# Performance work log

Hardware: AMD Instinct MI355X
Metric: run time of the kernel (lower is better)

## Reference

```python
import jax, jax.numpy as jnp
import numpy as np

NB, NG = 131072, 32768            # n_bus, n_gen nodes
EBB, EGB, EBG = 2097152, 65536, 65536  # bus-bus, gen->bus, bus->gen edges
CIN, C, COUT = 32, 64, 32         # in_channels, n_channels, out_channels
NL, NT = 2, 5                     # n_layers, n_taps+1
EPS = 1e-5


def setup_inputs() -> dict:
    key = jax.random.key(0)
    ks = iter(jax.random.split(key, 40))
    rn = lambda shape, s=1.0: jax.random.normal(next(ks), shape, dtype=jnp.float32) * s
    ri = lambda shape, hi: jax.random.randint(next(ks), shape, 0, hi, dtype=jnp.int32)
    inp = {
        'x_bus': rn((NB, CIN)), 'x_gen': rn((NG, CIN)),
        'readin_W_bus': rn((CIN, C), CIN ** -0.5), 'readin_b_bus': jnp.zeros((C,), jnp.float32),
        'readin_W_gen': rn((CIN, C), CIN ** -0.5), 'readin_b_gen': jnp.zeros((C,), jnp.float32),
        'bn_gamma_bus': jnp.ones((NL, C), jnp.float32), 'bn_beta_bus': jnp.zeros((NL, C), jnp.float32),
        'bn_gamma_gen': jnp.ones((NL, C), jnp.float32), 'bn_beta_gen': jnp.zeros((NL, C), jnp.float32),
        'taps_W_bus': rn((NL, NT, C, C), C ** -0.5), 'taps_b_bus': jnp.zeros((NL, NT, C), jnp.float32),
        'taps_W_gen': rn((NL, NT, C, C), C ** -0.5), 'taps_b_gen': jnp.zeros((NL, NT, C), jnp.float32),
        'readout_W_bus': rn((C, COUT), C ** -0.5), 'readout_b_bus': jnp.zeros((COUT,), jnp.float32),
        'readout_W_gen': rn((C, COUT), C ** -0.5), 'readout_b_gen': jnp.zeros((COUT,), jnp.float32),
        'edge_bb': ri((2, EBB), NB),
        'edge_gb_src': ri((EGB,), NG), 'edge_gb_dst': ri((EGB,), NB),
        'edge_bg_src': ri((EBG,), NB), 'edge_bg_dst': ri((EBG,), NG),
    }
    return inp


def _lrelu(v):
    return jnp.where(v >= 0, v, 0.01 * v)  # nn.LeakyReLU default slope


def _bn(v, g, b):
    # training-mode BatchNorm over the node dimension (biased variance)
    m = jnp.mean(v, axis=0)
    s = jnp.var(v, axis=0)
    return (v - m) * jax.lax.rsqrt(s + EPS) * g + b


def reference(x_bus, x_gen,
              readin_W_bus, readin_b_bus, readin_W_gen, readin_b_gen,
              bn_gamma_bus, bn_beta_bus, bn_gamma_gen, bn_beta_gen,
              taps_W_bus, taps_b_bus, taps_W_gen, taps_b_gen,
              readout_W_bus, readout_b_bus, readout_W_gen, readout_b_gen,
              edge_bb, edge_gb_src, edge_gb_dst, edge_bg_src, edge_bg_dst):
    seg = jax.ops.segment_sum
    bbs, bbd = edge_bb[0], edge_bb[1]
    # readin (single HeteroDictLinear, plain_last)
    xb = x_bus @ readin_W_bus + readin_b_bus   # [NB, C]
    xg = x_gen @ readin_W_gen + readin_b_gen   # [NG, C]
    for l in range(NL):  # residual blocks: norm -> act -> (dropout p=0) -> graph filter -> +x
        yb = _lrelu(_bn(xb, bn_gamma_bus[l], bn_beta_bus[l]))
        yg = _lrelu(_bn(xg, bn_gamma_gen[l], bn_beta_gen[l]))
        zb = yb @ taps_W_bus[l, 0] + taps_b_bus[l, 0]
        zg = yg @ taps_W_gen[l, 0] + taps_b_gen[l, 0]
        cb, cg = yb, yg
        for k in range(1, NT):  # graph shift (scatter-add over hetero edges) + per-type tap
            nb = seg(cb[bbs], bbd, num_segments=NB) + seg(cg[edge_gb_src], edge_gb_dst, num_segments=NB)
            ng = seg(cb[edge_bg_src], edge_bg_dst, num_segments=NG)
            cb, cg = nb, ng
            zb = zb + cb @ taps_W_bus[l, k] + taps_b_bus[l, k]
            zg = zg + cg @ taps_W_gen[l, k] + taps_b_gen[l, k]
        xb = xb + zb
        xg = xg + zg
    out_b = xb @ readout_W_bus + readout_b_bus  # [NB, COUT]
    out_g = xg @ readout_W_gen + readout_b_gen  # [NG, COUT]
    return (out_b, out_g)
```

## Files before the change

kernel.cpp:

```cpp
#include <hip/hip_runtime.h>

#define NBUS 131072
#define NGEN 32768
#define NALL (NBUS + NGEN)
#define NEBB 2097152
#define NEGB 65536
#define NEBG 65536
#define NEBUS (NEBB + NEGB)
#define NTILE (NALL / 64)
#define NTILE_BUS (NBUS / 64)

typedef float f32x2 __attribute__((ext_vector_type(2)));
typedef float f32x4 __attribute__((ext_vector_type(4)));
typedef short s16x8 __attribute__((ext_vector_type(8)));
typedef unsigned short u16;

__device__ inline f32x2 bf2x2(unsigned v) {
  f32x2 r;
  r.x = __builtin_bit_cast(float, v << 16);
  r.y = __builtin_bit_cast(float, v & 0xFFFF0000u);
  return r;
}
__device__ inline u16 f2bf(float f) {
  unsigned u = __builtin_bit_cast(unsigned, f);
  unsigned r = u + 0x7FFFu + ((u >> 16) & 1u);
  return (u16)(r >> 16);
}
__device__ inline unsigned pack2bf(float a, float b) {
  return (unsigned)f2bf(a) | ((unsigned)f2bf(b) << 16);
}

__global__ void __launch_bounds__(256) k_convw(const float* __restrict__ tWb,
                                               const float* __restrict__ tWg,
                                               const float* __restrict__ roWb,
                                               const float* __restrict__ roWg,
                                               const float* __restrict__ riWb,
                                               const float* __restrict__ riWg,
                                               u16* __restrict__ wt,
                                               u16* __restrict__ rot,
                                               u16* __restrict__ riwt) {
  int t = blockIdx.x * 256 + threadIdx.x;
  int S = gridDim.x * 256;
  for (int i = t; i < 20 * 4096; i += S) {
    int mat = i >> 12, off = i & 4095, n = off >> 6, k = off & 63;
    const float* src = (mat < 10) ? tWb : tWg;
    int tap = (mat < 10) ? mat : mat - 10;
    wt[i] = f2bf(src[(size_t)tap * 4096 + k * 64 + n]);
  }
  for (int i = t; i < 2 * 2048; i += S) {
    int type = i >> 11, off = i & 2047, n = off >> 6, k = off & 63;
    const float* src = type ? roWg : roWb;
    rot[i] = f2bf(src[k * 32 + n]);
  }
  for (int i = t; i < 2 * 2048; i += S) {
    int type = i >> 11, off = i & 2047, n = off >> 5, k = off & 31;
    const float* src = type ? riWg : riWb;
    riwt[i] = f2bf(src[k * 64 + n]);
  }
}

__global__ void __launch_bounds__(256) k_hist_sl(const int* __restrict__ bbDst,
                                                 const int* __restrict__ gbDst,
                                                 const int* __restrict__ bgDst,
                                                 int* __restrict__ busCnt,
                                                 int* __restrict__ bgCnt) {
  const int g = blockIdx.x & 7;
  const int blk = blockIdx.x >> 3;
  const int nblk = gridDim.x >> 3;
  const int start = blk * 256 + threadIdx.x;
  const int S = nblk * 256;
  int i = start;
  for (; i + 3 * S < NEBB; i += 4 * S) {
    int d0 = bbDst[i], d1 = bbDst[i + S], d2 = bbDst[i + 2 * S], d3 = bbDst[i + 3 * S];
    if ((d0 >> 14) == g) atomicAdd(&busCnt[d0], 1);
    if ((d1 >> 14) == g) atomicAdd(&busCnt[d1], 1);
    if ((d2 >> 14) == g) atomicAdd(&busCnt[d2], 1);
    if ((d3 >> 14) == g) atomicAdd(&busCnt[d3], 1);
  }
  for (; i < NEBB; i += S) {
    int d = bbDst[i];
    if ((d >> 14) == g) atomicAdd(&busCnt[d], 1);
  }
  for (i = start; i < NEGB; i += S) {
    int d = gbDst[i];
    if ((d >> 14) == g) atomicAdd(&busCnt[d], 1);
  }
  for (i = start; i < NEBG; i += S) {
    int d = bgDst[i];
    if ((d >> 12) == g) atomicAdd(&bgCnt[d], 1);
  }
}

__global__ void k_scan1(const int* __restrict__ in, int* __restrict__ out,
                        int* __restrict__ bsums, int n) {
  __shared__ int sh[256];
  int t = threadIdx.x;
  int base = blockIdx.x * 1024 + t * 4;
  int v0 = (base + 0 < n) ? in[base + 0] : 0;
  int v1 = (base + 1 < n) ? in[base + 1] : 0;
  int v2 = (base + 2 < n) ? in[base + 2] : 0;
  int v3 = (base + 3 < n) ? in[base + 3] : 0;
  int t0 = v0, t1 = t0 + v1, t2 = t1 + v2, t3 = t2 + v3;
  sh[t] = t3;
  __syncthreads();
  for (int off = 1; off < 256; off <<= 1) {
    int x = (t >= off) ? sh[t - off] : 0;
    __syncthreads();
    sh[t] += x;
    __syncthreads();
  }
  int excl = (t > 0) ? sh[t - 1] : 0;
  if (base + 0 < n) out[base + 0] = excl;
  if (base + 1 < n) out[base + 1] = excl + t0;
  if (base + 2 < n) out[base + 2] = excl + t1;
  if (base + 3 < n) out[base + 3] = excl + t2;
  if (t == 255) bsums[blockIdx.x] = sh[255];
}

__global__ void k_scan2(int* __restrict__ bsums, int nb) {
  __shared__ int sh[256];
  int t = threadIdx.x;
  int v = (t < nb) ? bsums[t] : 0;
  sh[t] = v;
  __syncthreads();
  for (int off = 1; off < 256; off <<= 1) {
    int x = (t >= off) ? sh[t - off] : 0;
    __syncthreads();
    sh[t] += x;
    __syncthreads();
  }
  int excl = (t > 0) ? sh[t - 1] : 0;
  if (t < nb) bsums[t] = excl;
}

__global__ void k_scan3(int* __restrict__ off, int* __restrict__ cur,
                        const int* __restrict__ bsums, int n, int E) {
  int stride = gridDim.x * blockDim.x;
  for (int i = blockIdx.x * blockDim.x + threadIdx.x; i < n; i += stride) {
    int o = off[i] + bsums[i >> 10];
    off[i] = o;
    cur[i] = o;
  }
  if (blockIdx.x == 0 && threadIdx.x == 0) off[n] = E;
}

__global__ void __launch_bounds__(256) k_fill_sl(const int* __restrict__ bbSrc,
                                                 const int* __restrict__ bbDst,
                                                 const int* __restrict__ gbSrc,
                                                 const int* __restrict__ gbDst,
                                                 const int* __restrict__ bgSrc,
                                                 const int* __restrict__ bgDst,
                                                 int* __restrict__ busCur,
                                                 int* __restrict__ bgCur,
                                                 int* __restrict__ busSrt,
                                                 int* __restrict__ bgSrt) {
  const int g = blockIdx.x & 7;
  const int tid = threadIdx.x;
  if (blockIdx.x < 2048) {
    const int blk = blockIdx.x >> 3;
    const int S = 256 * 256;
    int i = blk * 256 + tid;
    for (; i + 3 * S < NEBB; i += 4 * S) {
      int d0 = bbDst[i], d1 = bbDst[i + S], d2 = bbDst[i + 2 * S], d3 = bbDst[i + 3 * S];
      if ((d0 >> 14) == g) { int p = atomicAdd(&busCur[d0], 1); busSrt[p] = bbSrc[i]; }
      if ((d1 >> 14) == g) { int p = atomicAdd(&busCur[d1], 1); busSrt[p] = bbSrc[i + S]; }
      if ((d2 >> 14) == g) { int p = atomicAdd(&busCur[d2], 1); busSrt[p] = bbSrc[i + 2 * S]; }
      if ((d3 >> 14) == g) { int p = atomicAdd(&busCur[d3], 1); busSrt[p] = bbSrc[i + 3 * S]; }
    }
    for (; i < NEBB; i += S) {
      int d = bbDst[i];
      if ((d >> 14) == g) { int p = atomicAdd(&busCur[d], 1); busSrt[p] = bbSrc[i]; }
    }
  } else if (blockIdx.x < 2304) {
    const int blk = (blockIdx.x - 2048) >> 3;
    const int S = 32 * 256;
    for (int i = blk * 256 + tid; i < NEGB; i += S) {
      int d = gbDst[i];
      if ((d >> 14) == g) { int p = atomicAdd(&busCur[d], 1); busSrt[p] = gbSrc[i] + NBUS; }
    }
  } else {
    const int blk = (blockIdx.x - 2304) >> 3;
    const int S = 32 * 256;
    for (int i = blk * 256 + tid; i < NEBG; i += S) {
      int d = bgDst[i];
      if ((d >> 12) == g) { int p = atomicAdd(&bgCur[d], 1); bgSrt[p] = bgSrc[i]; }
    }
  }
}

__global__ void __launch_bounds__(256) k_readin(const float* __restrict__ xbus,
                                                const float* __restrict__ xgen,
                                                const u16* __restrict__ riwt,
                                                const float* __restrict__ bb_,
                                                const float* __restrict__ bg_,
                                                float* __restrict__ y,
                                                float* __restrict__ stats) {
  __shared__ float sst[128];
  const int tile = blockIdx.x;
  const bool isBus = tile < NTILE_BUS;
  const int tid = threadIdx.x, lane = tid & 63, wv = tid >> 6;
  const int m = lane & 15, kq = lane >> 4;
  const int grow = tile * 64 + wv * 16 + m;
  const float* xp = isBus ? &xbus[(size_t)grow * 32] : &xgen[(size_t)(grow - NBUS) * 32];
  s16x8 a;
#pragma unroll
  for (int j = 0; j < 8; j++) a[j] = (short)f2bf(xp[kq * 8 + j]);
  const u16* rb = riwt + (size_t)(isBus ? 0 : 1) * 2048;
  const float* bb = isBus ? bb_ : bg_;
  f32x4 acc[4];
#pragma unroll
  for (int cb = 0; cb < 4; cb++) {
    acc[cb] = (f32x4){0.f, 0.f, 0.f, 0.f};
    const u16* wp = rb + (cb * 16 + m) * 32 + kq * 8;
    s16x8 b = *(const s16x8*)wp;
    acc[cb] = __builtin_amdgcn_mfma_f32_16x16x32_bf16(a, b, acc[cb], 0, 0, 0);
  }
  if (tid < 128) sst[tid] = 0.f;
  __syncthreads();
  const int orow0 = tile * 64 + wv * 16 + kq * 4;
#pragma unroll
  for (int cb = 0; cb < 4; cb++) {
    int col = cb * 16 + m;
    float bv = bb[col];
    float s1 = 0.f, s2 = 0.f;
#pragma unroll
    for (int i = 0; i < 4; i++) {
      float yo = acc[cb][i] + bv;
      y[(size_t)(orow0 + i) * 64 + col] = yo;
      s1 += yo;
      s2 = fmaf(yo, yo, s2);
    }
    atomicAdd(&sst[col], s1);
    atomicAdd(&sst[64 + col], s2);
  }
  __syncthreads();
  if (tid < 64) {
    atomicAdd(&stats[(isBus ? 0 : 128) + tid], sst[tid]);
    atomicAdd(&stats[(isBus ? 0 : 128) + 64 + tid], sst[64 + tid]);
  }
}

__global__ void __launch_bounds__(256) k_norm_tap0(float* __restrict__ x,
                                                   u16* __restrict__ c0,
                                                   const float* __restrict__ stats,
                                                   const float* __restrict__ gammaB,
                                                   const float* __restrict__ betaB,
                                                   const float* __restrict__ gammaG,
                                                   const float* __restrict__ betaG,
                                                   const u16* __restrict__ wt,
                                                   const float* __restrict__ tbb,
                                                   const float* __restrict__ tbg,
                                                   int tapIdx) {
  __shared__ u16 yt[64][72];
  const int tile = blockIdx.x;
  const bool isBus = tile < NTILE_BUS;
  const int tid = threadIdx.x, lane = tid & 63, wv = tid >> 6;
  int so = isBus ? 0 : 128;
  float invN = isBus ? (1.0f / NBUS) : (1.0f / NGEN);
  float mn = stats[so + lane] * invN;
  float m2 = stats[so + 64 + lane] * invN;
  float rs = rsqrtf(m2 - mn * mn + 1e-5f);
  float scale = (isBus ? gammaB : gammaG)[lane] * rs;
  float shift = (isBus ? betaB : betaG)[lane] - mn * scale;
  unsigned* cu = (unsigned*)c0;
  int rw0 = tile * 64 + wv * 16;
  for (int i = 0; i < 16; i++) {
    int row = rw0 + i;
    float xv = x[(size_t)row * 64 + lane];
    float y = fmaf(xv, scale, shift);
    y = (y >= 0.f) ? y : 0.01f * y;
    float ypair = __shfl(y, lane ^ 1, 64);
    if ((lane & 1) == 0) {
      unsigned pk = pack2bf(y, ypair);
      cu[(size_t)row * 32 + (lane >> 1)] = pk;
      *(unsigned*)&yt[wv * 16 + i][lane] = pk;
    }
  }
  __syncthreads();
  const int m = lane & 15, kq = lane >> 4;
  const u16* wrow = wt + (size_t)((isBus ? 0 : 10) + tapIdx) * 4096;
  const float* bbase = isBus ? tbb : tbg;
  int lr = wv * 16 + m;
  s16x8 a0 = *(const s16x8*)&yt[lr][kq * 8];
  s16x8 a1 = *(const s16x8*)&yt[lr][32 + kq * 8];
  f32x4 acc[4];
#pragma unroll
  for (int cb = 0; cb < 4; cb++) acc[cb] = (f32x4){0.f, 0.f, 0.f, 0.f};
#pragma unroll
  for (int cb = 0; cb < 4; cb++) {
    const u16* wp = wrow + (cb * 16 + m) * 64 + kq * 8;
    s16x8 b0 = *(const s16x8*)&wp[0];
    s16x8 b1 = *(const s16x8*)&wp[32];
    acc[cb] = __builtin_amdgcn_mfma_f32_16x16x32_bf16(a0, b0, acc[cb], 0, 0, 0);
    acc[cb] = __builtin_amdgcn_mfma_f32_16x16x32_bf16(a1, b1, acc[cb], 0, 0, 0);
  }
  const int orow0 = tile * 64 + wv * 16 + kq * 4;
#pragma unroll
  for (int cb = 0; cb < 4; cb++) {
    int col = cb * 16 + m;
    float bsv = bbase[(size_t)tapIdx * 64 + col];
#pragma unroll
    for (int i = 0; i < 4; i++) {
      size_t idx = (size_t)(orow0 + i) * 64 + col;
      x[idx] += acc[cb][i] + bsv;
    }
  }
}

__global__ void __launch_bounds__(256) k_gather(const int* __restrict__ busOff,
                                                const int* __restrict__ busSrt,
                                                const int* __restrict__ bgOff,
                                                const int* __restrict__ bgSrt,
                                                const u16* __restrict__ src,
                                                u16* __restrict__ dst) {
  const int lane = threadIdx.x & 63;
  const int wv = threadIdx.x >> 6;
  const int grp = lane >> 3;
  const int sub = lane & 7;
  const unsigned* s32 = (const unsigned*)src;
  unsigned* d32 = (unsigned*)dst;
  int rowBase = (blockIdx.x * 4 + wv) * 8;
  const int rstride = gridDim.x * 32;
  for (int row0 = rowBase; row0 < NALL; row0 += rstride) {
    int row = row0 + grp;
    int beg, end;
    const int* srt;
    if (row < NBUS) {
      beg = busOff[row];
      end = busOff[row + 1];
      srt = busSrt;
    } else {
      beg = bgOff[row - NBUS];
      end = bgOff[row - NBUS + 1];
      srt = bgSrt;
    }
    f32x2 a0 = {0.f, 0.f}, a1 = {0.f, 0.f}, a2 = {0.f, 0.f}, a3 = {0.f, 0.f};
    for (int e = beg; e < end; e += 8) {
      uint4 v[8];
      int last = end - 1;
#pragma unroll
      for (int j = 0; j < 8; j++) {
        int idx = e + j;
        bool ok = idx < end;
        if (!ok) idx = last;
        int s = srt[idx];
        uint4 vv = *(const uint4*)&s32[(size_t)s * 32 + sub * 4];
        if (!ok) { vv.x = 0; vv.y = 0; vv.z = 0; vv.w = 0; }
        v[j] = vv;
      }
#pragma unroll
      for (int j = 0; j < 8; j++) {
        a0 += bf2x2(v[j].x);
        a1 += bf2x2(v[j].y);
        a2 += bf2x2(v[j].z);
        a3 += bf2x2(v[j].w);
      }
    }
    uint4 o;
    o.x = pack2bf(a0.x, a0.y);
    o.y = pack2bf(a1.x, a1.y);
    o.z = pack2bf(a2.x, a2.y);
    o.w = pack2bf(a3.x, a3.y);
    *(uint4*)&d32[(size_t)row * 32 + sub * 4] = o;
  }
}

__global__ void __launch_bounds__(256) k_tap2(const u16* __restrict__ cA,
                                              const u16* __restrict__ cB,
                                              float* __restrict__ x,
                                              const u16* __restrict__ wt,
                                              const float* __restrict__ tbb,
                                              const float* __restrict__ tbg,
                                              int idxA, int idxB,
                                              float* __restrict__ stats) {
  __shared__ float sst[128];
  const int tile = blockIdx.x;
  const bool isBus = tile < NTILE_BUS;
  const int row0 = tile * 64;
  const int tid = threadIdx.x, lane = tid & 63, wv = tid >> 6;
  const int m = lane & 15, kq = lane >> 4;
  const int arow = row0 + wv * 16 + m;
  const float* bbase = isBus ? tbb : tbg;
  const u16* wbase = wt + (size_t)(isBus ? 0 : 10) * 4096;
  f32x4 acc[4];
#pragma unroll
  for (int cb = 0; cb < 4; cb++) acc[cb] = (f32x4){0.f, 0.f, 0.f, 0.f};
  const u16* cs[2] = {cA, cB};
  const int idxs[2] = {idxA, idxB};
#pragma unroll
  for (int s = 0; s < 2; s++) {
    const u16* c = cs[s];
    s16x8 a0 = *(const s16x8*)&c[(size_t)arow * 64 + kq * 8];
    s16x8 a1 = *(const s16x8*)&c[(size_t)arow * 64 + 32 + kq * 8];
    const u16* wrow = wbase + (size_t)idxs[s] * 4096;
#pragma unroll
    for (int cb = 0; cb < 4; cb++) {
      const u16* wp = wrow + (cb * 16 + m) * 64 + kq * 8;
      s16x8 b0 = *(const s16x8*)&wp[0];
      s16x8 b1 = *(const s16x8*)&wp[32];
      acc[cb] = __builtin_amdgcn_mfma_f32_16x16x32_bf16(a0, b0, acc[cb], 0, 0, 0);
      acc[cb] = __builtin_amdgcn_mfma_f32_16x16x32_bf16(a1, b1, acc[cb], 0, 0, 0);
    }
  }
  if (stats) {
    if (tid < 128) sst[tid] = 0.f;
    __syncthreads();
  }
  const int orow0 = row0 + wv * 16 + kq * 4;
#pragma unroll
  for (int cb = 0; cb < 4; cb++) {
    int col = cb * 16 + m;
    float bsv = bbase[(size_t)idxA * 64 + col] + bbase[(size_t)idxB * 64 + col];
    float s1 = 0.f, s2 = 0.f;
#pragma unroll
    for (int i = 0; i < 4; i++) {
      size_t idx = (size_t)(orow0 + i) * 64 + col;
      float xo = x[idx] + acc[cb][i] + bsv;
      x[idx] = xo;
      s1 += xo;
      s2 = fmaf(xo, xo, s2);
    }
    if (stats) {
      atomicAdd(&sst[col], s1);
      atomicAdd(&sst[64 + col], s2);
    }
  }
  if (stats) {
    __syncthreads();
    if (tid < 64) {
      atomicAdd(&stats[(isBus ? 0 : 128) + tid], sst[tid]);
      atomicAdd(&stats[(isBus ? 0 : 128) + 64 + tid], sst[64 + tid]);
    }
  }
}

__global__ void __launch_bounds__(256) k_readout(const float* __restrict__ x,
                                                 const u16* __restrict__ rot,
                                                 const float* __restrict__ robb,
                                                 const float* __restrict__ robg,
                                                 float* __restrict__ out) {
  const int tile = blockIdx.x;
  const bool isBus = tile < NTILE_BUS;
  const int tid = threadIdx.x, lane = tid & 63, wv = tid >> 6;
  const int m = lane & 15, kq = lane >> 4;
  const int arow = tile * 64 + wv * 16 + m;
  const float* xp = &x[(size_t)arow * 64 + kq * 8];
  s16x8 a0, a1;
#pragma unroll
  for (int j = 0; j < 8; j++) a0[j] = (short)f2bf(xp[j]);
#pragma unroll
  for (int j = 0; j < 8; j++) a1[j] = (short)f2bf(xp[32 + j]);
  const u16* rbase = rot + (size_t)(isBus ? 0 : 1) * 2048;
  f32x4 acc[2];
  acc[0] = (f32x4){0.f, 0.f, 0.f, 0.f};
  acc[1] = (f32x4){0.f, 0.f, 0.f, 0.f};
#pragma unroll
  for (int cb = 0; cb < 2; cb++) {
    const u16* wp = rbase + (cb * 16 + m) * 64 + kq * 8;
    s16x8 b0 = *(const s16x8*)&wp[0];
    s16x8 b1 = *(const s16x8*)&wp[32];
    acc[cb] = __builtin_amdgcn_mfma_f32_16x16x32_bf16(a0, b0, acc[cb], 0, 0, 0);
    acc[cb] = __builtin_amdgcn_mfma_f32_16x16x32_bf16(a1, b1, acc[cb], 0, 0, 0);
  }
  const float* bb = isBus ? robb : robg;
  const int orow0 = tile * 64 + wv * 16 + kq * 4;
#pragma unroll
  for (int cb = 0; cb < 2; cb++) {
    int col = cb * 16 + m;
    float bv = bb[col];
#pragma unroll
    for (int i = 0; i < 4; i++)
      out[(size_t)(orow0 + i) * 32 + col] = acc[cb][i] + bv;
  }
}

extern "C" void kernel_launch(void* const* d_in, const int* in_sizes, int n_in,
                              void* d_out, int out_size, void* d_ws, size_t ws_size,
                              hipStream_t stream) {
  const float* x_bus = (const float*)d_in[0];
  const float* x_gen = (const float*)d_in[1];
  const float* riWb = (const float*)d_in[2];
  const float* ribb = (const float*)d_in[3];
  const float* riWg = (const float*)d_in[4];
  const float* ribg = (const float*)d_in[5];
  const float* bng_b = (const float*)d_in[6];
  const float* bnb_b = (const float*)d_in[7];
  const float* bng_g = (const float*)d_in[8];
  const float* bnb_g = (const float*)d_in[9];
  const float* tWb = (const float*)d_in[10];
  const float* tbb = (const float*)d_in[11];
  const float* tWg = (const float*)d_in[12];
  const float* tbg = (const float*)d_in[13];
  const float* roWb = (const float*)d_in[14];
  const float* robb = (const float*)d_in[15];
  const float* roWg = (const float*)d_in[16];
  const float* robg = (const float*)d_in[17];
  const int* ebb = (const int*)d_in[18];
  const int* gb_src = (const int*)d_in[19];
  const int* gb_dst = (const int*)d_in[20];
  const int* bg_src = (const int*)d_in[21];
  const int* bg_dst = (const int*)d_in[22];
  const int* bb_src = ebb;
  const int* bb_dst = ebb + NEBB;

  char* p = (char*)d_ws;
  auto take = [&](size_t bytes) -> void* {
    void* r = (void*)p;
    p += (bytes + 255) & ~(size_t)255;
    return r;
  };
  float* x = (float*)take((size_t)NALL * 64 * 4);
  u16* b0 = (u16*)take((size_t)NALL * 64 * 2);
  u16* b1 = (u16*)take((size_t)NALL * 64 * 2);
  u16* b2 = (u16*)take((size_t)NALL * 64 * 2);
  int* bus_off = (int*)take((size_t)(NBUS + 1) * 4);
  int* bus_srt = (int*)take((size_t)NEBUS * 4);
  int* bg_off = (int*)take((size_t)(NGEN + 1) * 4);
  int* bg_srt = (int*)take((size_t)NEBG * 4);
  int* bsums = (int*)take(256 * 4);
  u16* wt = (u16*)take((size_t)20 * 4096 * 2);
  u16* rot = (u16*)take((size_t)2 * 2048 * 2);
  u16* riwt = (u16*)take((size_t)2 * 2048 * 2);
  int* bus_cur = (int*)take((size_t)NBUS * 4);
  int* bg_cur = (int*)take((size_t)NGEN * 4);
  float* stats0 = (float*)take(256 * 4);
  float* stats1 = (float*)take(256 * 4);
  size_t zlen = (char*)p - (char*)bus_cur;
  if ((size_t)(p - (char*)d_ws) > ws_size) return;

  hipMemsetAsync(bus_cur, 0, zlen, stream);
  k_convw<<<320, 256, 0, stream>>>(tWb, tWg, roWb, roWg, riWb, riWg, wt, rot, riwt);

  k_hist_sl<<<2048, 256, 0, stream>>>(bb_dst, gb_dst, bg_dst, bus_cur, bg_cur);

  k_scan1<<<128, 256, 0, stream>>>(bus_cur, bus_off, bsums, NBUS);
  k_scan2<<<1, 256, 0, stream>>>(bsums, 128);
  k_scan3<<<512, 256, 0, stream>>>(bus_off, bus_cur, bsums, NBUS, NEBUS);

  k_scan1<<<32, 256, 0, stream>>>(bg_cur, bg_off, bsums, NGEN);
  k_scan2<<<1, 256, 0, stream>>>(bsums, 32);
  k_scan3<<<128, 256, 0, stream>>>(bg_off, bg_cur, bsums, NGEN, NEBG);

  k_fill_sl<<<2560, 256, 0, stream>>>(bb_src, bb_dst, gb_src, gb_dst, bg_src, bg_dst,
                                      bus_cur, bg_cur, bus_srt, bg_srt);

  k_readin<<<NTILE, 256, 0, stream>>>(x_bus, x_gen, riwt, ribb, ribg, x, stats0);

  for (int l = 0; l < 2; l++) {
    float* statsL = (l == 0) ? stats0 : stats1;
    k_norm_tap0<<<NTILE, 256, 0, stream>>>(x, b0, statsL,
                                           bng_b + l * 64, bnb_b + l * 64,
                                           bng_g + l * 64, bnb_g + l * 64,
                                           wt, tbb, tbg, l * 5);
    k_gather<<<2560, 256, 0, stream>>>(bus_off, bus_srt, bg_off, bg_srt, b0, b1);
    k_gather<<<2560, 256, 0, stream>>>(bus_off, bus_srt, bg_off, bg_srt, b1, b2);
    k_tap2<<<NTILE, 256, 0, stream>>>(b1, b2, x, wt, tbb, tbg,
                                      l * 5 + 1, l * 5 + 2, (float*)nullptr);
    k_gather<<<2560, 256, 0, stream>>>(bus_off, bus_srt, bg_off, bg_srt, b2, b0);
    k_gather<<<2560, 256, 0, stream>>>(bus_off, bus_srt, bg_off, bg_srt, b0, b1);
    k_tap2<<<NTILE, 256, 0, stream>>>(b0, b1, x, wt, tbb, tbg,
                                      l * 5 + 3, l * 5 + 4,
                                      (l == 0) ? stats1 : (float*)nullptr);
  }

  k_readout<<<NTILE, 256, 0, stream>>>(x, rot, robb, robg, (float*)d_out);
}
```

Before: 839.4 us.

## Merge independent kernels into combined launches and share gather indices via shuffles

Independent stages now run inside one launch, split by block index: histogram with readin, both scans, CSR fill with the layer-0 norm, and the third gather with the tap2 that consumes the previous two gathers. This removes launch gaps and lets latency-bound work overlap with compute-bound work. The gather now loads one edge index per lane and broadcasts it with __shfl instead of having every lane reload all eight indices. The combined kernels carry more code and may use more registers, and they rely on the fused halves touching disjoint buffers.

```diff
diff --git a/kernel.cpp b/kernel.cpp
--- a/kernel.cpp
+++ b/kernel.cpp
@@ -9,6 +9,7 @@
 #define NEBUS (NEBB + NEGB)
 #define NTILE (NALL / 64)
 #define NTILE_BUS (NBUS / 64)
+#define NGB 2560
 
 typedef float f32x2 __attribute__((ext_vector_type(2)));
 typedef float f32x4 __attribute__((ext_vector_type(4)));
@@ -59,16 +60,14 @@
   }
 }
 
-__global__ void __launch_bounds__(256) k_hist_sl(const int* __restrict__ bbDst,
-                                                 const int* __restrict__ gbDst,
-                                                 const int* __restrict__ bgDst,
-                                                 int* __restrict__ busCnt,
-                                                 int* __restrict__ bgCnt) {
-  const int g = blockIdx.x & 7;
-  const int blk = blockIdx.x >> 3;
-  const int nblk = gridDim.x >> 3;
+__device__ inline void dev_hist(int bid, const int* __restrict__ bbDst,
+                                const int* __restrict__ gbDst,
+                                const int* __restrict__ bgDst,
+                                int* __restrict__ busCnt, int* __restrict__ bgCnt) {
+  const int g = bid & 7;
+  const int blk = bid >> 3;
   const int start = blk * 256 + threadIdx.x;
-  const int S = nblk * 256;
+  const int S = 256 * 256;
   int i = start;
   for (; i + 3 * S < NEBB; i += 4 * S) {
     int d0 = bbDst[i], d1 = bbDst[i + S], d2 = bbDst[i + 2 * S], d3 = bbDst[i + 3 * S];
@@ -91,11 +90,73 @@
   }
 }
 
-__global__ void k_scan1(const int* __restrict__ in, int* __restrict__ out,
-                        int* __restrict__ bsums, int n) {
+__device__ inline void dev_readin(int tile, const float* __restrict__ xbus,
+                                  const float* __restrict__ xgen,
+                                  const u16* __restrict__ riwt,
+                                  const float* __restrict__ bb_,
+                                  const float* __restrict__ bg_,
+                                  float* __restrict__ y, float* __restrict__ stats) {
+  __shared__ float sst[128];
+  const bool isBus = tile < NTILE_BUS;
+  const int tid = threadIdx.x, lane = tid & 63, wv = tid >> 6;
+  const int m = lane & 15, kq = lane >> 4;
+  const int grow = tile * 64 + wv * 16 + m;
+  const float* xp = isBus ? &xbus[(size_t)grow * 32] : &xgen[(size_t)(grow - NBUS) * 32];
+  s16x8 a;
+#pragma unroll
+  for (int j = 0; j < 8; j++) a[j] = (short)f2bf(xp[kq * 8 + j]);
+  const u16* rb = riwt + (size_t)(isBus ? 0 : 1) * 2048;
+  const float* bb = isBus ? bb_ : bg_;
+  f32x4 acc[4];
+#pragma unroll
+  for (int cb = 0; cb < 4; cb++) {
+    acc[cb] = (f32x4){0.f, 0.f, 0.f, 0.f};
+    const u16* wp = rb + (cb * 16 + m) * 32 + kq * 8;
+    s16x8 b = *(const s16x8*)wp;
+    acc[cb] = __builtin_amdgcn_mfma_f32_16x16x32_bf16(a, b, acc[cb], 0, 0, 0);
+  }
+  if (tid < 128) sst[tid] = 0.f;
+  __syncthreads();
+  const int orow0 = tile * 64 + wv * 16 + kq * 4;
+#pragma unroll
+  for (int cb = 0; cb < 4; cb++) {
+    int col = cb * 16 + m;
+    float bv = bb[col];
+    float s1 = 0.f, s2 = 0.f;
+#pragma unroll
+    for (int i = 0; i < 4; i++) {
+      float yo = acc[cb][i] + bv;
+      y[(size_t)(orow0 + i) * 64 + col] = yo;
+      s1 += yo;
+      s2 = fmaf(yo, yo, s2);
+    }
+    atomicAdd(&sst[col], s1);
+    atomicAdd(&sst[64 + col], s2);
+  }
+  __syncthreads();
+  if (tid < 64) {
+    atomicAdd(&stats[(isBus ? 0 : 128) + tid], sst[tid]);
+    atomicAdd(&stats[(isBus ? 0 : 128) + 64 + tid], sst[64 + tid]);
+  }
+}
+
+__global__ void __launch_bounds__(256) k_hist_readin(
+    const int* __restrict__ bbDst, const int* __restrict__ gbDst,
+    const int* __restrict__ bgDst, int* __restrict__ busCnt, int* __restrict__ bgCnt,
+    const float* __restrict__ xbus, const float* __restrict__ xgen,
+    const u16* __restrict__ riwt, const float* __restrict__ bb_,
+    const float* __restrict__ bg_, float* __restrict__ y, float* __restrict__ stats) {
+  if (blockIdx.x < 2048)
+    dev_hist(blockIdx.x, bbDst, gbDst, bgDst, busCnt, bgCnt);
+  else
+    dev_readin(blockIdx.x - 2048, xbus, xgen, riwt, bb_, bg_, y, stats);
+}
+
+__device__ inline void dev_scan1(int bid, const int* __restrict__ in,
+                                 int* __restrict__ out, int* __restrict__ bsums, int n) {
   __shared__ int sh[256];
   int t = threadIdx.x;
-  int base = blockIdx.x * 1024 + t * 4;
+  int base = bid * 1024 + t * 4;
   int v0 = (base + 0 < n) ? in[base + 0] : 0;
   int v1 = (base + 1 < n) ? in[base + 1] : 0;
   int v2 = (base + 2 < n) ? in[base + 2] : 0;
@@ -114,10 +175,19 @@
   if (base + 1 < n) out[base + 1] = excl + t0;
   if (base + 2 < n) out[base + 2] = excl + t1;
   if (base + 3 < n) out[base + 3] = excl + t2;
-  if (t == 255) bsums[blockIdx.x] = sh[255];
-}
-
-__global__ void k_scan2(int* __restrict__ bsums, int nb) {
+  if (t == 255) bsums[bid] = sh[255];
+}
+
+__global__ void k_scanA(const int* __restrict__ busCnt, int* __restrict__ busOff,
+                        int* __restrict__ bsums, const int* __restrict__ bgCnt,
+                        int* __restrict__ bgOff, int* __restrict__ bsums2) {
+  if (blockIdx.x < 128)
+    dev_scan1(blockIdx.x, busCnt, busOff, bsums, NBUS);
+  else
+    dev_scan1(blockIdx.x - 128, bgCnt, bgOff, bsums2, NGEN);
+}
+
+__device__ inline void dev_scan2(int* __restrict__ bsums, int nb) {
   __shared__ int sh[256];
   int t = threadIdx.x;
   int v = (t < nb) ? bsums[t] : 0;
@@ -133,31 +203,46 @@
   if (t < nb) bsums[t] = excl;
 }
 
-__global__ void k_scan3(int* __restrict__ off, int* __restrict__ cur,
-                        const int* __restrict__ bsums, int n, int E) {
-  int stride = gridDim.x * blockDim.x;
-  for (int i = blockIdx.x * blockDim.x + threadIdx.x; i < n; i += stride) {
+__global__ void k_scanB(int* __restrict__ bsums, int* __restrict__ bsums2) {
+  if (blockIdx.x == 0)
+    dev_scan2(bsums, 128);
+  else
+    dev_scan2(bsums2, 32);
+}
+
+__device__ inline void dev_scan3(int bid, int nblk, int* __restrict__ off,
+                                 int* __restrict__ cur, const int* __restrict__ bsums,
+                                 int n, int E) {
+  int stride = nblk * 256;
+  for (int i = bid * 256 + threadIdx.x; i < n; i += stride) {
     int o = off[i] + bsums[i >> 10];
     off[i] = o;
     cur[i] = o;
   }
-  if (blockIdx.x == 0 && threadIdx.x == 0) off[n] = E;
-}
-
-__global__ void __launch_bounds__(256) k_fill_sl(const int* __restrict__ bbSrc,
-                                                 const int* __restrict__ bbDst,
-                                                 const int* __restrict__ gbSrc,
-                                                 const int* __restrict__ gbDst,
-                                                 const int* __restrict__ bgSrc,
-                                                 const int* __restrict__ bgDst,
-                                                 int* __restrict__ busCur,
-                                                 int* __restrict__ bgCur,
-                                                 int* __restrict__ busSrt,
-                                                 int* __restrict__ bgSrt) {
-  const int g = blockIdx.x & 7;
+  if (bid == 0 && threadIdx.x == 0) off[n] = E;
+}
+
+__global__ void k_scanC(int* __restrict__ busOff, int* __restrict__ busCur,
+                        const int* __restrict__ bsums, int* __restrict__ bgOff,
+                        int* __restrict__ bgCur, const int* __restrict__ bsums2) {
+  if (blockIdx.x < 512)
+    dev_scan3(blockIdx.x, 512, busOff, busCur, bsums, NBUS, NEBUS);
+  else
+    dev_scan3(blockIdx.x - 512, 128, bgOff, bgCur, bsums2, NGEN, NEBG);
+}
+
+__device__ inline void dev_fill(int bid, const int* __restrict__ bbSrc,
+                                const int* __restrict__ bbDst,
+                                const int* __restrict__ gbSrc,
+                                const int* __restrict__ gbDst,
+                                const int* __restrict__ bgSrc,
+                                const int* __restrict__ bgDst,
+                                int* __restrict__ busCur, int* __restrict__ bgCur,
+                                int* __restrict__ busSrt, int* __restrict__ bgSrt) {
+  const int g = bid & 7;
   const int tid = threadIdx.x;
-  if (blockIdx.x < 2048) {
-    const int blk = blockIdx.x >> 3;
+  if (bid < 2048) {
+    const int blk = bid >> 3;
     const int S = 256 * 256;
     int i = blk * 256 + tid;
     for (; i + 3 * S < NEBB; i += 4 * S) {
@@ -171,15 +256,15 @@
       int d = bbDst[i];
       if ((d >> 14) == g) { int p = atomicAdd(&busCur[d], 1); busSrt[p] = bbSrc[i]; }
     }
-  } else if (blockIdx.x < 2304) {
-    const int blk = (blockIdx.x - 2048) >> 3;
+  } else if (bid < 2304) {
+    const int blk = (bid - 2048) >> 3;
     const int S = 32 * 256;
     for (int i = blk * 256 + tid; i < NEGB; i += S) {
       int d = gbDst[i];
       if ((d >> 14) == g) { int p = atomicAdd(&busCur[d], 1); busSrt[p] = gbSrc[i] + NBUS; }
     }
   } else {
-    const int blk = (blockIdx.x - 2304) >> 3;
+    const int blk = (bid - 2304) >> 3;
     const int S = 32 * 256;
     for (int i = blk * 256 + tid; i < NEBG; i += S) {
       int d = bgDst[i];
@@ -188,71 +273,16 @@
   }
 }
 
-__global__ void __launch_bounds__(256) k_readin(const float* __restrict__ xbus,
-                                                const float* __restrict__ xgen,
-                                                const u16* __restrict__ riwt,
-                                                const float* __restrict__ bb_,
-                                                const float* __restrict__ bg_,
-                                                float* __restrict__ y,
-                                                float* __restrict__ stats) {
-  __shared__ float sst[128];
-  const int tile = blockIdx.x;
-  const bool isBus = tile < NTILE_BUS;
-  const int tid = threadIdx.x, lane = tid & 63, wv = tid >> 6;
-  const int m = lane & 15, kq = lane >> 4;
-  const int grow = tile * 64 + wv * 16 + m;
-  const float* xp = isBus ? &xbus[(size_t)grow * 32] : &xgen[(size_t)(grow - NBUS) * 32];
-  s16x8 a;
-#pragma unroll
-  for (int j = 0; j < 8; j++) a[j] = (short)f2bf(xp[kq * 8 + j]);
-  const u16* rb = riwt + (size_t)(isBus ? 0 : 1) * 2048;
-  const float* bb = isBus ? bb_ : bg_;
-  f32x4 acc[4];
-#pragma unroll
-  for (int cb = 0; cb < 4; cb++) {
-    acc[cb] = (f32x4){0.f, 0.f, 0.f, 0.f};
-    const u16* wp = rb + (cb * 16 + m) * 32 + kq * 8;
-    s16x8 b = *(const s16x8*)wp;
-    acc[cb] = __builtin_amdgcn_mfma_f32_16x16x32_bf16(a, b, acc[cb], 0, 0, 0);
-  }
-  if (tid < 128) sst[tid] = 0.f;
-  __syncthreads();
-  const int orow0 = tile * 64 + wv * 16 + kq * 4;
-#pragma unroll
-  for (int cb = 0; cb < 4; cb++) {
-    int col = cb * 16 + m;
-    float bv = bb[col];
-    float s1 = 0.f, s2 = 0.f;
-#pragma unroll
-    for (int i = 0; i < 4; i++) {
-      float yo = acc[cb][i] + bv;
-      y[(size_t)(orow0 + i) * 64 + col] = yo;
-      s1 += yo;
-      s2 = fmaf(yo, yo, s2);
-    }
-    atomicAdd(&sst[col], s1);
-    atomicAdd(&sst[64 + col], s2);
-  }
-  __syncthreads();
-  if (tid < 64) {
-    atomicAdd(&stats[(isBus ? 0 : 128) + tid], sst[tid]);
-    atomicAdd(&stats[(isBus ? 0 : 128) + 64 + tid], sst[64 + tid]);
-  }
-}
-
-__global__ void __launch_bounds__(256) k_norm_tap0(float* __restrict__ x,
-                                                   u16* __restrict__ c0,
-                                                   const float* __restrict__ stats,
-                                                   const float* __restrict__ gammaB,
-                                                   const float* __restrict__ betaB,
-                                                   const float* __restrict__ gammaG,
-                                                   const float* __restrict__ betaG,
-                                                   const u16* __restrict__ wt,
-                                                   const float* __restrict__ tbb,
-                                                   const float* __restrict__ tbg,
-                                                   int tapIdx) {
+__device__ inline void dev_norm(int tile, float* __restrict__ x, u16* __restrict__ c0,
+                                const float* __restrict__ stats,
+                                const float* __restrict__ gammaB,
+                                const float* __restrict__ betaB,
+                                const float* __restrict__ gammaG,
+                                const float* __restrict__ betaG,
+                                const u16* __restrict__ wt,
+                                const float* __restrict__ tbb,
+                                const float* __restrict__ tbg, int tapIdx) {
   __shared__ u16 yt[64][72];
-  const int tile = blockIdx.x;
   const bool isBus = tile < NTILE_BUS;
   const int tid = threadIdx.x, lane = tid & 63, wv = tid >> 6;
   int so = isBus ? 0 : 128;
@@ -307,21 +337,49 @@
   }
 }
 
-__global__ void __launch_bounds__(256) k_gather(const int* __restrict__ busOff,
-                                                const int* __restrict__ busSrt,
-                                                const int* __restrict__ bgOff,
-                                                const int* __restrict__ bgSrt,
-                                                const u16* __restrict__ src,
-                                                u16* __restrict__ dst) {
+__global__ void __launch_bounds__(256) k_fill_norm(
+    const int* __restrict__ bbSrc, const int* __restrict__ bbDst,
+    const int* __restrict__ gbSrc, const int* __restrict__ gbDst,
+    const int* __restrict__ bgSrc, const int* __restrict__ bgDst,
+    int* __restrict__ busCur, int* __restrict__ bgCur,
+    int* __restrict__ busSrt, int* __restrict__ bgSrt,
+    float* __restrict__ x, u16* __restrict__ c0, const float* __restrict__ stats,
+    const float* __restrict__ gammaB, const float* __restrict__ betaB,
+    const float* __restrict__ gammaG, const float* __restrict__ betaG,
+    const u16* __restrict__ wt, const float* __restrict__ tbb,
+    const float* __restrict__ tbg, int tapIdx) {
+  if (blockIdx.x < 2560)
+    dev_fill(blockIdx.x, bbSrc, bbDst, gbSrc, gbDst, bgSrc, bgDst,
+             busCur, bgCur, busSrt, bgSrt);
+  else
+    dev_norm(blockIdx.x - 2560, x, c0, stats, gammaB, betaB, gammaG, betaG,
+             wt, tbb, tbg, tapIdx);
+}
+
+__global__ void __launch_bounds__(256) k_norm(
+    float* __restrict__ x, u16* __restrict__ c0, const float* __restrict__ stats,
+    const float* __restrict__ gammaB, const float* __restrict__ betaB,
+    const float* __restrict__ gammaG, const float* __restrict__ betaG,
+    const u16* __restrict__ wt, const float* __restrict__ tbb,
+    const float* __restrict__ tbg, int tapIdx) {
+  dev_norm(blockIdx.x, x, c0, stats, gammaB, betaB, gammaG, betaG,
+           wt, tbb, tbg, tapIdx);
+}
+
+__device__ inline void dev_gather(int bid, const int* __restrict__ busOff,
+                                  const int* __restrict__ busSrt,
+                                  const int* __restrict__ bgOff,
+                                  const int* __restrict__ bgSrt,
+                                  const u16* __restrict__ src, u16* __restrict__ dst) {
   const int lane = threadIdx.x & 63;
   const int wv = threadIdx.x >> 6;
   const int grp = lane >> 3;
   const int sub = lane & 7;
+  const int gb = grp << 3;
   const unsigned* s32 = (const unsigned*)src;
   unsigned* d32 = (unsigned*)dst;
-  int rowBase = (blockIdx.x * 4 + wv) * 8;
-  const int rstride = gridDim.x * 32;
-  for (int row0 = rowBase; row0 < NALL; row0 += rstride) {
+  int rowBase = (bid * 4 + wv) * 8;
+  for (int row0 = rowBase; row0 < NALL; row0 += NGB * 32) {
     int row = row0 + grp;
     int beg, end;
     const int* srt;
@@ -335,17 +393,16 @@
       srt = bgSrt;
     }
     f32x2 a0 = {0.f, 0.f}, a1 = {0.f, 0.f}, a2 = {0.f, 0.f}, a3 = {0.f, 0.f};
+    int last = end - 1;
     for (int e = beg; e < end; e += 8) {
+      int ei = e + sub;
+      int sv = srt[ei <= last ? ei : last];
       uint4 v[8];
-      int last = end - 1;
 #pragma unroll
       for (int j = 0; j < 8; j++) {
-        int idx = e + j;
-        bool ok = idx < end;
-        if (!ok) idx = last;
-        int s = srt[idx];
+        int s = __shfl(sv, gb + j, 64);
         uint4 vv = *(const uint4*)&s32[(size_t)s * 32 + sub * 4];
-        if (!ok) { vv.x = 0; vv.y = 0; vv.z = 0; vv.w = 0; }
+        if (e + j > last) { vv.x = 0; vv.y = 0; vv.z = 0; vv.w = 0; }
         v[j] = vv;
       }
 #pragma unroll
@@ -362,6 +419,81 @@
     o.z = pack2bf(a2.x, a2.y);
     o.w = pack2bf(a3.x, a3.y);
     *(uint4*)&d32[(size_t)row * 32 + sub * 4] = o;
+  }
+}
+
+__global__ void __launch_bounds__(256) k_gather(const int* __restrict__ busOff,
+                                                const int* __restrict__ busSrt,
+                                                const int* __restrict__ bgOff,
+                                                const int* __restrict__ bgSrt,
+                                                const u16* __restrict__ src,
+                                                u16* __restrict__ dst) {
+  dev_gather(blockIdx.x, busOff, busSrt, bgOff, bgSrt, src, dst);
+}
+
+__device__ inline void dev_tap2(int tile, const u16* __restrict__ cA,
+                                const u16* __restrict__ cB, float* __restrict__ x,
+                                const u16* __restrict__ wt,
+                                const float* __restrict__ tbb,
+                                const float* __restrict__ tbg,
+                                int idxA, int idxB, float* __restrict__ stats) {
+  __shared__ float sst[128];
+  const bool isBus = tile < NTILE_BUS;
+  const int row0 = tile * 64;
+  const int tid = threadIdx.x, lane = tid & 63, wv = tid >> 6;
+  const int m = lane & 15, kq = lane >> 4;
+  const int arow = row0 + wv * 16 + m;
+  const float* bbase = isBus ? tbb : tbg;
+  const u16* wbase = wt + (size_t)(isBus ? 0 : 10) * 4096;
+  f32x4 acc[4];
+#pragma unroll
+  for (int cb = 0; cb < 4; cb++) acc[cb] = (f32x4){0.f, 0.f, 0.f, 0.f};
+  const u16* cs[2] = {cA, cB};
+  const int idxs[2] = {idxA, idxB};
+#pragma unroll
+  for (int s = 0; s < 2; s++) {
+    const u16* c = cs[s];
+    s16x8 a0 = *(const s16x8*)&c[(size_t)arow * 64 + kq * 8];
+    s16x8 a1 = *(const s16x8*)&c[(size_t)arow * 64 + 32 + kq * 8];
+    const u16* wrow = wbase + (size_t)idxs[s] * 4096;
+#pragma unroll
+    for (int cb = 0; cb < 4; cb++) {
+      const u16* wp = wrow + (cb * 16 + m) * 64 + kq * 8;
+      s16x8 b0 = *(const s16x8*)&wp[0];
+      s16x8 b1 = *(const s16x8*)&wp[32];
+      acc[cb] = __builtin_amdgcn_mfma_f32_16x16x32_bf16(a0, b0, acc[cb], 0, 0, 0);
+      acc[cb] = __builtin_amdgcn_mfma_f32_16x16x32_bf16(a1, b1, acc[cb], 0, 0, 0);
+    }
+  }
+  if (stats) {
+    if (tid < 128) sst[tid] = 0.f;
+    __syncthreads();
+  }
+  const int orow0 = row0 + wv * 16 + kq * 4;
+#pragma unroll
+  for (int cb = 0; cb < 4; cb++) {
+    int col = cb * 16 + m;
+    float bsv = bbase[(size_t)idxA * 64 + col] + bbase[(size_t)idxB * 64 + col];
+    float s1 = 0.f, s2 = 0.f;
+#pragma unroll
+    for (int i = 0; i < 4; i++) {
+      size_t idx = (size_t)(orow0 + i) * 64 + col;
+      float xo = x[idx] + acc[cb][i] + bsv;
+      x[idx] = xo;
+      s1 += xo;
+      s2 = fmaf(xo, xo, s2);
+    }
+    if (stats) {
+      atomicAdd(&sst[col], s1);
+      atomicAdd(&sst[64 + col], s2);
+    }
+  }
+  if (stats) {
+    __syncthreads();
+    if (tid < 64) {
+      atomicAdd(&stats[(isBus ? 0 : 128) + tid], sst[tid]);
+      atomicAdd(&stats[(isBus ? 0 : 128) + 64 + tid], sst[64 + tid]);
+    }
   }
 }
 
@@ -373,65 +505,20 @@
                                               const float* __restrict__ tbg,
                                               int idxA, int idxB,
                                               float* __restrict__ stats) {
-  __shared__ float sst[128];
-  const int tile = blockIdx.x;
-  const bool isBus = tile < NTILE_BUS;
-  const int row0 = tile * 64;
-  const int tid = threadIdx.x, lane = tid & 63, wv = tid >> 6;
-  const int m = lane & 15, kq = lane >> 4;
-  const int arow = row0 + wv * 16 + m;
-  const float* bbase = isBus ? tbb : tbg;
-  const u16* wbase = wt + (size_t)(isBus ? 0 : 10) * 4096;
-  f32x4 acc[4];
-#pragma unroll
-  for (int cb = 0; cb < 4; cb++) acc[cb] = (f32x4){0.f, 0.f, 0.f, 0.f};
-  const u16* cs[2] = {cA, cB};
-  const int idxs[2] = {idxA, idxB};
-#pragma unroll
-  for (int s = 0; s < 2; s++) {
-    const u16* c = cs[s];
-    s16x8 a0 = *(const s16x8*)&c[(size_t)arow * 64 + kq * 8];
-    s16x8 a1 = *(const s16x8*)&c[(size_t)arow * 64 + 32 + kq * 8];
-    const u16* wrow = wbase + (size_t)idxs[s] * 4096;
-#pragma unroll
-    for (int cb = 0; cb < 4; cb++) {
-      const u16* wp = wrow + (cb * 16 + m) * 64 + kq * 8;
-      s16x8 b0 = *(const s16x8*)&wp[0];
-      s16x8 b1 = *(const s16x8*)&wp[32];
-      acc[cb] = __builtin_amdgcn_mfma_f32_16x16x32_bf16(a0, b0, acc[cb], 0, 0, 0);
-      acc[cb] = __builtin_amdgcn_mfma_f32_16x16x32_bf16(a1, b1, acc[cb], 0, 0, 0);
-    }
-  }
-  if (stats) {
-    if (tid < 128) sst[tid] = 0.f;
-    __syncthreads();
-  }
-  const int orow0 = row0 + wv * 16 + kq * 4;
-#pragma unroll
-  for (int cb = 0; cb < 4; cb++) {
-    int col = cb * 16 + m;
-    float bsv = bbase[(size_t)idxA * 64 + col] + bbase[(size_t)idxB * 64 + col];
-    float s1 = 0.f, s2 = 0.f;
-#pragma unroll
-    for (int i = 0; i < 4; i++) {
-      size_t idx = (size_t)(orow0 + i) * 64 + col;
-      float xo = x[idx] + acc[cb][i] + bsv;
-      x[idx] = xo;
-      s1 += xo;
-      s2 = fmaf(xo, xo, s2);
-    }
-    if (stats) {
-      atomicAdd(&sst[col], s1);
-      atomicAdd(&sst[64 + col], s2);
-    }
-  }
-  if (stats) {
-    __syncthreads();
-    if (tid < 64) {
-      atomicAdd(&stats[(isBus ? 0 : 128) + tid], sst[tid]);
-      atomicAdd(&stats[(isBus ? 0 : 128) + 64 + tid], sst[64 + tid]);
-    }
-  }
+  dev_tap2(blockIdx.x, cA, cB, x, wt, tbb, tbg, idxA, idxB, stats);
+}
+
+__global__ void __launch_bounds__(256) k_gather_tap2(
+    const int* __restrict__ busOff, const int* __restrict__ busSrt,
+    const int* __restrict__ bgOff, const int* __restrict__ bgSrt,
+    const u16* __restrict__ gsrc, u16* __restrict__ gdst,
+    const u16* __restrict__ cA, const u16* __restrict__ cB, float* __restrict__ x,
+    const u16* __restrict__ wt, const float* __restrict__ tbb,
+    const float* __restrict__ tbg, int idxA, int idxB) {
+  if (blockIdx.x < NGB)
+    dev_gather(blockIdx.x, busOff, busSrt, bgOff, bgSrt, gsrc, gdst);
+  else
+    dev_tap2(blockIdx.x - NGB, cA, cB, x, wt, tbb, tbg, idxA, idxB, (float*)nullptr);
 }
 
 __global__ void __launch_bounds__(256) k_readout(const float* __restrict__ x,
@@ -518,6 +605,7 @@
   int* bg_off = (int*)take((size_t)(NGEN + 1) * 4);
   int* bg_srt = (int*)take((size_t)NEBG * 4);
   int* bsums = (int*)take(256 * 4);
+  int* bsums2 = (int*)take(256 * 4);
   u16* wt = (u16*)take((size_t)20 * 4096 * 2);
   u16* rot = (u16*)take((size_t)2 * 2048 * 2);
   u16* riwt = (u16*)take((size_t)2 * 2048 * 2);
@@ -531,35 +619,29 @@
   hipMemsetAsync(bus_cur, 0, zlen, stream);
   k_convw<<<320, 256, 0, stream>>>(tWb, tWg, roWb, roWg, riWb, riWg, wt, rot, riwt);
 
-  k_hist_sl<<<2048, 256, 0, stream>>>(bb_dst, gb_dst, bg_dst, bus_cur, bg_cur);
-
-  k_scan1<<<128, 256, 0, stream>>>(bus_cur, bus_off, bsums, NBUS);
-  k_scan2<<<1, 256, 0, stream>>>(bsums, 128);
-  k_scan3<<<512, 256, 0, stream>>>(bus_off, bus_cur, bsums, NBUS, NEBUS);
-
-  k_scan1<<<32, 256, 0, stream>>>(bg_cur, bg_off, bsums, NGEN);
-  k_scan2<<<1, 256, 0, stream>>>(bsums, 32);
-  k_scan3<<<128, 256, 0, stream>>>(bg_off, bg_cur, bsums, NGEN, NEBG);
-
-  k_fill_sl<<<2560, 256, 0, stream>>>(bb_src, bb_dst, gb_src, gb_dst, bg_src, bg_dst,
-                                      bus_cur, bg_cur, bus_srt, bg_srt);
-
-  k_readin<<<NTILE, 256, 0, stream>>>(x_bus, x_gen, riwt, ribb, ribg, x, stats0);
+  k_hist_readin<<<4608, 256, 0, stream>>>(bb_dst, gb_dst, bg_dst, bus_cur, bg_cur,
+                                          x_bus, x_gen, riwt, ribb, ribg, x, stats0);
+
+  k_scanA<<<160, 256, 0, stream>>>(bus_cur, bus_off, bsums, bg_cur, bg_off, bsums2);
+  k_scanB<<<2, 256, 0, stream>>>(bsums, bsums2);
+  k_scanC<<<640, 256, 0, stream>>>(bus_off, bus_cur, bsums, bg_off, bg_cur, bsums2);
+
+  k_fill_norm<<<5120, 256, 0, stream>>>(bb_src, bb_dst, gb_src, gb_dst, bg_src, bg_dst,
+                                        bus_cur, bg_cur, bus_srt, bg_srt,
+                                        x, b0, stats0, bng_b, bnb_b, bng_g, bnb_g,
+                                        wt, tbb, tbg, 0);
 
   for (int l = 0; l < 2; l++) {
-    float* statsL = (l == 0) ? stats0 : stats1;
-    k_norm_tap0<<<NTILE, 256, 0, stream>>>(x, b0, statsL,
-                                           bng_b + l * 64, bnb_b + l * 64,
-                                           bng_g + l * 64, bnb_g + l * 64,
-                                           wt, tbb, tbg, l * 5);
-    k_gather<<<2560, 256, 0, stream>>>(bus_off, bus_srt, bg_off, bg_srt, b0, b1);
-    k_gather<<<2560, 256, 0, stream>>>(bus_off, bus_srt, bg_off, bg_srt, b1, b2);
-    k_tap2<<<NTILE, 256, 0, stream>>>(b1, b2, x, wt, tbb, tbg,
-                                      l * 5 + 1, l * 5 + 2, (float*)nullptr);
-    k_gather<<<2560, 256, 0, stream>>>(bus_off, bus_srt, bg_off, bg_srt, b2, b0);
-    k_gather<<<2560, 256, 0, stream>>>(bus_off, bus_srt, bg_off, bg_srt, b0, b1);
-    k_tap2<<<NTILE, 256, 0, stream>>>(b0, b1, x, wt, tbb, tbg,
-                                      l * 5 + 3, l * 5 + 4,
+    if (l == 1)
+      k_norm<<<NTILE, 256, 0, stream>>>(x, b0, stats1, bng_b + 64, bnb_b + 64,
+                                        bng_g + 64, bnb_g + 64, wt, tbb, tbg, 5);
+    k_gather<<<NGB, 256, 0, stream>>>(bus_off, bus_srt, bg_off, bg_srt, b0, b1);
+    k_gather<<<NGB, 256, 0, stream>>>(bus_off, bus_srt, bg_off, bg_srt, b1, b2);
+    k_gather_tap2<<<NGB + NTILE, 256, 0, stream>>>(bus_off, bus_srt, bg_off, bg_srt,
+                                                   b2, b0, b1, b2, x, wt, tbb, tbg,
+                                                   l * 5 + 1, l * 5 + 2);
+    k_gather<<<NGB, 256, 0, stream>>>(bus_off, bus_srt, bg_off, bg_srt, b0, b1);
+    k_tap2<<<NTILE, 256, 0, stream>>>(b0, b1, x, wt, tbb, tbg, l * 5 + 3, l * 5 + 4,
                                       (l == 0) ? stats1 : (float*)nullptr);
   }
 
```

Result: no change. 826.6 us (-1.5%).
